# Performance work log

Hardware: AMD Instinct MI355X
Metric: run time of the kernel (lower is better)

The kernel has to match this reference:

```python
import jax, jax.numpy as jnp
import numpy as np

EPS = 1e-5
COMMIT_W = 2.0
LATENT = 64


def _conv1d(x, w, b, stride, padding):
    # x: [B,C,T], w: [O,I,K] (torch Conv1d layout)
    y = jax.lax.conv_general_dilated(x, w, (stride,), [(padding, padding)],
                                     dimension_numbers=('NCH', 'OIH', 'NCH'))
    return y + b[None, :, None]


def _bn(x, g, b):
    # training-mode BatchNorm1d: batch statistics over (B, T) per channel
    mu = x.mean(axis=(0, 2), keepdims=True)
    var = x.var(axis=(0, 2), keepdims=True)
    return (x - mu) * jax.lax.rsqrt(var + EPS) * g[None, :, None] + b[None, :, None]


def setup_inputs():
    key = jax.random.key(0)
    ks = jax.random.split(key, 10)
    B, T, D, K = 8, 10240, LATENT, 8192
    f32 = jnp.float32
    def n(k, shape, scale):
        return jax.random.normal(k, shape, dtype=f32) * scale
    return {
        'x': jax.random.normal(ks[0], (B, 1, T), dtype=f32),
        'enc_w1': n(ks[1], (16, 1, 5), 0.3), 'enc_b1': jnp.zeros((16,), f32),
        'bn1_g': jnp.ones((16,), f32), 'bn1_b': jnp.zeros((16,), f32),
        'enc_w2': n(ks[2], (32, 16, 5), 0.1), 'enc_b2': jnp.zeros((32,), f32),
        'bn2_g': jnp.ones((32,), f32), 'bn2_b': jnp.zeros((32,), f32),
        'enc_w3': n(ks[3], (64, 32, 25), 0.05), 'enc_b3': jnp.zeros((64,), f32),
        'bn3_g': jnp.ones((64,), f32), 'bn3_b': jnp.zeros((64,), f32),
        'codebook': jax.random.normal(ks[4], (K, D), dtype=f32),
        'dec_wt': n(ks[5], (64, 64, 25), 0.05),  # torch ConvTranspose1d [in,out,k]
        'dbn1_g': jnp.ones((64,), f32), 'dbn1_b': jnp.zeros((64,), f32),
        'dec_w2': n(ks[6], (64, 64, 5), 0.08), 'dec_b2': jnp.zeros((64,), f32),
        'dbn2_g': jnp.ones((64,), f32), 'dbn2_b': jnp.zeros((64,), f32),
        'dec_w3': n(ks[7], (1, 64, 1), 0.1), 'dec_b3': jnp.zeros((1,), f32),
    }


def reference(x, enc_w1, enc_b1, bn1_g, bn1_b, enc_w2, enc_b2, bn2_g, bn2_b,
              enc_w3, enc_b3, bn3_g, bn3_b, codebook, dec_wt, dbn1_g, dbn1_b,
              dec_w2, dec_b2, dbn2_g, dbn2_b, dec_w3, dec_b3):
    # ---- encoder ----
    h = jax.nn.silu(_conv1d(x, enc_w1, enc_b1, 1, 2))
    h = _bn(h, bn1_g, bn1_b)
    h = jax.nn.silu(_conv1d(h, enc_w2, enc_b2, 1, 2))
    h = _bn(h, bn2_g, bn2_b)
    h = jnp.tanh(_conv1d(h, enc_w3, enc_b3, 5, 12))
    z = _bn(h, bn3_g, bn3_b)                       # [B, 64, L]
    B, _, L = z.shape
    # ---- VQ: euclidean nearest-neighbor against codebook ----
    zf = z.transpose(0, 2, 1).reshape(-1, LATENT)  # [N, D]
    d = ((zf * zf).sum(-1, keepdims=True)
         - 2.0 * zf @ codebook.T
         + (codebook * codebook).sum(-1)[None, :])  # [N, K]
    idx = jnp.argmin(d, axis=-1)                   # [N]
    q = codebook[idx]                              # [N, D]
    commit_loss = COMMIT_W * jnp.mean((jax.lax.stop_gradient(q) - zf) ** 2)
    q_st = zf + jax.lax.stop_gradient(q - zf)      # straight-through
    zq = q_st.reshape(B, L, LATENT).transpose(0, 2, 1)  # [B, 64, L]
    # ---- decoder ----
    # ConvTranspose1d(k=25, s=5, p=12) == dilated conv with flipped kernel
    wconv = jnp.flip(dec_wt, -1).transpose(1, 0, 2)     # [out, in, k]
    h = jax.lax.conv_general_dilated(zq, wconv, (1,), [(12, 12)], lhs_dilation=(5,),
                                     dimension_numbers=('NCH', 'OIH', 'NCH'))
    h = jax.nn.silu(h)
    h = _bn(h, dbn1_g, dbn1_b)
    h = jax.nn.silu(_conv1d(h, dec_w2, dec_b2, 1, 2))
    h = _bn(h, dbn2_g, dbn2_b)
    recon = _conv1d(h, dec_w3, dec_b3, 1, 0)       # [B, 1, ~T]
    T = x.shape[2]
    cur = recon.shape[2]
    if cur > T:
        recon = recon[:, :, :T]
    elif cur < T:
        recon = jnp.pad(recon, ((0, 0), (0, 0), (0, T - cur)))
    return recon, idx.reshape(B, L), commit_loss
```

## Files before the change

### kernel.cpp

```cpp
#include <hip/hip_runtime.h>
#include <hip/hip_bf16.h>

#define DEV __device__ __forceinline__

typedef __attribute__((ext_vector_type(8))) short s8v;
typedef __attribute__((ext_vector_type(16))) float f32x16;
typedef __attribute__((address_space(1))) const unsigned int u32g;
typedef __attribute__((address_space(3))) unsigned int u32l;

DEV void gl_lds(const void* g, void* l){
  __builtin_amdgcn_global_load_lds((u32g*)g, (u32l*)l, 16, 0, 0);
}

DEV float siluf(float x){ return x / (1.f + expf(-x)); }

DEV float wredsum(float v){
  #pragma unroll
  for(int m = 32; m; m >>= 1) v += __shfl_xor(v, m);
  return v;
}

DEV unsigned short bf16rne(float f){
  unsigned int u = __float_as_uint(f);
  u += 0x7FFFu + ((u >> 16) & 1u);
  return (unsigned short)(u >> 16);
}
DEV float bf16tof(unsigned short h){ return __uint_as_float(((unsigned int)h) << 16); }

DEV unsigned umed3(unsigned a, unsigned b, unsigned c){
  unsigned d;
  asm("v_med3_u32 %0, %1, %2, %3" : "=v"(d) : "v"(a), "v"(b), "v"(c));
  return d;
}

#define S1 0
#define Q1 16
#define S2 32
#define Q2 64
#define S3 96
#define Q3 160
#define S4 224
#define Q4 288
#define S5 352
#define Q5 416
#define SLOSS 480
#define NSTATF 512

#define EPSQ 6u
#define NCHUNK 8

__global__ void k_prep(const float* ew3, const float* dwt, float* w3t, float* dwtt,
                       unsigned short* wb7){
  const int n1 = 64*32*25, n2 = 64*64*25;
  for(int i = blockIdx.x*blockDim.x + threadIdx.x; i < n1+n2; i += gridDim.x*blockDim.x){
    if(i < n1){
      int c = i/(32*25), r = i - c*(32*25), ii = r/25, k = r - ii*25;
      w3t[(ii*25 + k)*64 + c] = ew3[i];
    } else {
      int j = i - n1;
      int ii = j/(64*25), r = j - ii*(64*25), o = r/25, k = r - o*25;
      float w = dwt[j];
      dwtt[(ii*25 + k)*64 + o] = w;
      wb7[((size_t)(k*64 + o))*64 + ii] = bf16rne(w);
    }
  }
}

__global__ void k_prep2(const float* __restrict__ cb, unsigned short* __restrict__ cbsw,
                        float* __restrict__ cnw, float* __restrict__ cnw2,
                        unsigned short* __restrict__ cbb, int* cnt){
  if(blockIdx.x == 0 && threadIdx.x == 0) *cnt = 0;
  int j = blockIdx.x*256 + threadIdx.x;
  if(j < 8192){
    float nrm = 0.f;
    unsigned swz = (j & 15) << 4;
    char* rowp = (char*)cbsw + (size_t)j*256;
    #pragma unroll
    for(int k = 0; k < 64; k++){
      float x = cb[(size_t)j*64 + k];
      unsigned short hi = bf16rne(x);
      float lo = x - bf16tof(hi);
      *(unsigned short*)(rowp + (((unsigned)(2*k)) ^ swz)) = hi;
      *(unsigned short*)(rowp + (((unsigned)(128 + 2*k)) ^ swz)) = bf16rne(lo);
      cbb[(size_t)j*64 + k] = hi;
      nrm = fmaf(x, x, nrm);
    }
    cnw[j] = nrm;
    cnw2[j] = (nrm + 1024.f) * 256.f;
  }
}

__global__ void k1(const float* __restrict__ x, const float* __restrict__ w1,
                   const float* __restrict__ b1, float* __restrict__ h1, float* stats){
  __shared__ float xs[260];
  __shared__ float ssum[16], ssq[16];
  int tid = threadIdx.x, b = blockIdx.y, t0 = blockIdx.x*256;
  if(tid < 16){ ssum[tid] = 0.f; ssq[tid] = 0.f; }
  for(int i = tid; i < 260; i += 256){
    int t = t0 + i - 2;
    xs[i] = (t >= 0 && t < 10240) ? x[b*10240 + t] : 0.f;
  }
  __syncthreads();
  int t = t0 + tid;
  #pragma unroll
  for(int c = 0; c < 16; c++){
    float a = b1[c];
    #pragma unroll
    for(int k = 0; k < 5; k++) a = fmaf(w1[c*5+k], xs[tid+k], a);
    a = siluf(a);
    h1[((b*16 + c)*10240) + t] = a;
    float s = wredsum(a), s2 = wredsum(a*a);
    if((tid & 63) == 0){ atomicAdd(&ssum[c], s); atomicAdd(&ssq[c], s2); }
  }
  __syncthreads();
  if(tid < 16){ atomicAdd(stats+S1+tid, ssum[tid]); atomicAdd(stats+Q1+tid, ssq[tid]); }
}

__global__ void k2(const float* __restrict__ h1, const float* __restrict__ w2,
                   const float* __restrict__ b2, const float* __restrict__ g1,
                   const float* __restrict__ bb1, float* __restrict__ h2out, float* stats){
  __shared__ float hs[16*264];
  __shared__ float wl[2560];
  __shared__ float A1[16], B1[16];
  __shared__ float ssum[32], ssq[32];
  int tid = threadIdx.x, b = blockIdx.y, t0 = blockIdx.x*256;
  for(int i = tid; i < 2560; i += 256) wl[i] = w2[i];
  if(tid < 16){
    float mu = stats[S1+tid]/81920.f;
    float var = stats[Q1+tid]/81920.f - mu*mu;
    float rs = rsqrtf(var + 1e-5f);
    A1[tid] = rs*g1[tid];
    B1[tid] = bb1[tid] - mu*rs*g1[tid];
  }
  if(tid < 32){ ssum[tid] = 0.f; ssq[tid] = 0.f; }
  __syncthreads();
  for(int i = tid; i < 16*260; i += 256){
    int ch = i/260, tt = i - ch*260;
    int t = t0 + tt - 2;
    hs[ch*264 + tt] = (t >= 0 && t < 10240) ? (h1[((b*16+ch)*10240)+t]*A1[ch] + B1[ch]) : 0.f;
  }
  __syncthreads();
  int t = t0 + tid;
  float acc[32];
  #pragma unroll
  for(int c = 0; c < 32; c++) acc[c] = b2[c];
  for(int i = 0; i < 16; i++){
    float z0 = hs[i*264+tid], z1 = hs[i*264+tid+1], z2 = hs[i*264+tid+2],
          z3 = hs[i*264+tid+3], z4 = hs[i*264+tid+4];
    #pragma unroll
    for(int c = 0; c < 32; c++){
      const float* wp = &wl[(c*16+i)*5];
      acc[c] = fmaf(wp[0],z0,fmaf(wp[1],z1,fmaf(wp[2],z2,fmaf(wp[3],z3,fmaf(wp[4],z4,acc[c])))));
    }
  }
  #pragma unroll
  for(int c = 0; c < 32; c++){
    float a = siluf(acc[c]);
    h2out[((b*32 + c)*10240) + t] = a;
    float s = wredsum(a), s2 = wredsum(a*a);
    if((tid & 63) == 0){ atomicAdd(&ssum[c], s); atomicAdd(&ssq[c], s2); }
  }
  __syncthreads();
  if(tid < 32){ atomicAdd(stats+S2+tid, ssum[tid]); atomicAdd(stats+Q2+tid, ssq[tid]); }
}

__global__ void k3(const float* __restrict__ h2, const float* __restrict__ w3t,
                   const float* __restrict__ eb3, const float* __restrict__ g2,
                   const float* __restrict__ bb2, float* __restrict__ zn, float* stats){
  __shared__ float X[5*32*40];
  __shared__ float A2[32], B2[32];
  __shared__ float ssum[64], ssq[64];
  int tid = threadIdx.x, b = blockIdx.y, l0 = blockIdx.x*32;
  if(tid < 32){
    float mu = stats[S2+tid]/81920.f;
    float var = stats[Q2+tid]/81920.f - mu*mu;
    float rs = rsqrtf(var + 1e-5f);
    A2[tid] = rs*g2[tid];
    B2[tid] = bb2[tid] - mu*rs*g2[tid];
  }
  if(tid < 64){ ssum[tid] = 0.f; ssq[tid] = 0.f; }
  __syncthreads();
  for(int i2 = tid; i2 < 5*32*36; i2 += 256){
    int kk = i2/(32*36);
    int r  = i2 - kk*(32*36);
    int ch = r/36, m = r - ch*36;
    int t = 5*(l0 + m) + kk - 12;
    float v = 0.f;
    if(t >= 0 && t < 10240) v = h2[((b*32+ch)*10240)+t]*A2[ch] + B2[ch];
    X[(kk*32+ch)*40 + m] = v;
  }
  __syncthreads();
  int c = tid & 63, lslot = tid >> 6;
  float acc[8];
  float bias = eb3[c];
  #pragma unroll
  for(int s = 0; s < 8; s++) acc[s] = bias;
  for(int i = 0; i < 32; i++){
    #pragma unroll
    for(int kk = 0; kk < 5; kk++){
      float z[12];
      #pragma unroll
      for(int j = 0; j < 12; j++) z[j] = X[(kk*32+i)*40 + lslot*8 + j];
      #pragma unroll
      for(int kap = 0; kap < 5; kap++){
        float w = w3t[(i*25 + kap*5 + kk)*64 + c];
        #pragma unroll
        for(int s = 0; s < 8; s++) acc[s] = fmaf(w, z[s+kap], acc[s]);
      }
    }
  }
  float ls = 0.f, lq = 0.f;
  #pragma unroll
  for(int s = 0; s < 8; s++){
    int l = l0 + lslot*8 + s;
    float a = tanhf(acc[s]);
    zn[((b*2048 + l)*64) + c] = a;
    ls += a; lq += a*a;
  }
  atomicAdd(&ssum[c], ls); atomicAdd(&ssq[c], lq);
  __syncthreads();
  if(tid < 64){ atomicAdd(stats+S3+tid, ssum[tid]); atomicAdd(stats+Q3+tid, ssq[tid]); }
}

__global__ void k3b(float* zn, const float* g3, const float* b3, const float* stats){
  __shared__ float A[64], B[64];
  int tid = threadIdx.x;
  if(tid < 64){
    float mu = stats[S3+tid]/16384.f;
    float var = stats[Q3+tid]/16384.f - mu*mu;
    float rs = rsqrtf(var + 1e-5f);
    A[tid] = rs*g3[tid];
    B[tid] = b3[tid] - mu*rs*g3[tid];
  }
  __syncthreads();
  for(int i = blockIdx.x*256 + tid; i < 16384*64; i += gridDim.x*256){
    int c = i & 63;
    zn[i] = zn[i]*A[c] + B[c];
  }
}

__global__ __launch_bounds__(256, 3) void k5m(const float* __restrict__ zn,
    const unsigned short* __restrict__ cbsw, const float* __restrict__ cnw2,
    unsigned int* __restrict__ pbk, unsigned int* __restrict__ psk){
  __shared__ __align__(16) unsigned char cbuf[2][16384];
  __shared__ unsigned int redb[64][2], reds[64][2];
  int tid = threadIdx.x;
  int chunk = blockIdx.x;
  int m0 = blockIdx.y * 64;
  int lane = tid & 63, widx = tid >> 6;
  int wr = widx >> 1, wc = widx & 1;
  int h = lane >> 5;
  int row = m0 + wr*32 + (lane & 31);

  s8v ah[4], al[4];
  const float* zp = zn + (size_t)row*64;
  #pragma unroll
  for(int s = 0; s < 4; s++){
    float4 v0 = *(const float4*)(zp + s*16 + h*8);
    float4 v1 = *(const float4*)(zp + s*16 + h*8 + 4);
    float vv[8] = {v0.x,v0.y,v0.z,v0.w,v1.x,v1.y,v1.z,v1.w};
    #pragma unroll
    for(int i = 0; i < 8; i++){
      unsigned short hi = bf16rne(vv[i]);
      ah[s][i] = (short)hi;
      al[s][i] = (short)bf16rne(vv[i] - bf16tof(hi));
    }
  }

  unsigned int bk[16], sk[16];
  #pragma unroll
  for(int r = 0; r < 16; r++){ bk[r] = 0xFFFFFFFFu; sk[r] = 0xFFFFFFFFu; }
  f32x16 zv;
  #pragma unroll
  for(int i = 0; i < 16; i++) zv[i] = 0.f;

  int c0 = chunk * 1024;
  const char* csrc = (const char*)cbsw + (size_t)c0*256;
  #pragma unroll
  for(int c2 = 0; c2 < 4; c2++)
    gl_lds(csrc + c2*4096 + tid*16, &cbuf[0][0] + c2*4096 + tid*16);
  __syncthreads();

  int cl = wc*32 + (lane & 31);
  unsigned swz = (unsigned)(cl & 15) << 4;
  unsigned col = (unsigned)(c0 + cl);
  for(int tile = 0; tile < 16; ++tile){
    int bsel = tile & 1;
    if(tile < 15){
      const char* ns = csrc + (size_t)(tile+1)*16384;
      #pragma unroll
      for(int c2 = 0; c2 < 4; c2++)
        gl_lds(ns + c2*4096 + tid*16, &cbuf[bsel^1][0] + c2*4096 + tid*16);
    }
    const unsigned char* bp = &cbuf[bsel][0] + cl*256;
    s8v bh[4], bl[4];
    #pragma unroll
    for(int s = 0; s < 4; s++){
      bh[s] = *(const s8v*)(bp + (((unsigned)(s*32 + h*16)) ^ swz));
      bl[s] = *(const s8v*)(bp + (((unsigned)(128 + s*32 + h*16)) ^ swz));
    }
    float cnv2 = cnw2[col];
    f32x16 a1 = __builtin_amdgcn_mfma_f32_32x32x16_bf16(ah[0], bh[0], zv, 0, 0, 0);
    f32x16 a2 = __builtin_amdgcn_mfma_f32_32x32x16_bf16(al[0], bh[0], zv, 0, 0, 0);
    a2 = __builtin_amdgcn_mfma_f32_32x32x16_bf16(ah[0], bl[0], a2, 0, 0, 0);
    #pragma unroll
    for(int s = 1; s < 4; s++){
      a1 = __builtin_amdgcn_mfma_f32_32x32x16_bf16(ah[s], bh[s], a1, 0, 0, 0);
      a2 = __builtin_amdgcn_mfma_f32_32x32x16_bf16(al[s], bh[s], a2, 0, 0, 0);
      a2 = __builtin_amdgcn_mfma_f32_32x32x16_bf16(ah[s], bl[s], a2, 0, 0, 0);
    }
    #pragma unroll
    for(int r = 0; r < 16; r++){
      float q = fmaf(-512.f, a1[r], cnv2);
      q = fmaf(-512.f, a2[r], q);
      q = fminf(q, 524287.f);
      unsigned k = (((unsigned)q) << 13) | col;
      unsigned nb = bk[r] < k ? bk[r] : k;
      sk[r] = umed3(sk[r], bk[r], k);
      bk[r] = nb;
    }
    col += 64;
    __syncthreads();
  }

  #pragma unroll
  for(int m = 1; m <= 16; m <<= 1){
    #pragma unroll
    for(int r = 0; r < 16; r++){
      unsigned int ob = (unsigned int)__shfl_xor((int)bk[r], m);
      unsigned int os = (unsigned int)__shfl_xor((int)sk[r], m);
      unsigned int s2 = sk[r] < os ? sk[r] : os;
      sk[r] = umed3(s2, bk[r], ob);
      bk[r] = bk[r] < ob ? bk[r] : ob;
    }
  }
  if((lane & 31) == 0){
    #pragma unroll
    for(int r = 0; r < 16; r++){
      int lr = wr*32 + (r&3) + 8*(r>>2) + 4*h;
      redb[lr][wc] = bk[r]; reds[lr][wc] = sk[r];
    }
  }
  __syncthreads();
  if(tid < 64){
    unsigned int b0 = redb[tid][0], b1v = redb[tid][1];
    unsigned int s0 = reds[tid][0], s1v = reds[tid][1];
    unsigned int ss = s0 < s1v ? s0 : s1v;
    ss = umed3(ss, b0, b1v);
    unsigned int bb = b0 < b1v ? b0 : b1v;
    size_t o = (size_t)chunk*16384 + m0 + tid;
    pbk[o] = bb;
    psk[o] = ss;
  }
}

__global__ void k5r(const unsigned int* __restrict__ pbk,
                    const unsigned int* __restrict__ psk, int* __restrict__ idxw,
                    float* __restrict__ out_idx, int* __restrict__ list, int* cnt){
  int row = blockIdx.x*256 + threadIdx.x;
  unsigned int bk = pbk[row], sk = psk[row];
  #pragma unroll
  for(int c = 1; c < NCHUNK; c++){
    unsigned int ob = pbk[(size_t)c*16384 + row];
    unsigned int os = psk[(size_t)c*16384 + row];
    unsigned int s2 = sk < os ? sk : os;
    sk = umed3(s2, bk, ob);
    bk = bk < ob ? bk : ob;
  }
  int idx = (int)(bk & 0x1FFFu);
  idxw[row] = idx;
  out_idx[row] = (float)idx;
  if((sk >> 13) - (bk >> 13) <= EPSQ){
    int p = atomicAdd(cnt, 1);
    list[p] = row;
  }
}

__global__ __launch_bounds__(256) void k5x(const float* __restrict__ zn,
    const float* __restrict__ cb, const float* __restrict__ cnw,
    const int* __restrict__ list, const int* cnt,
    float* __restrict__ pxd, int* __restrict__ pxi){
  int tid = threadIdx.x;
  int chunk = blockIdx.x;
  int n = *cnt;
  int rgrp = tid >> 6, cs = tid & 63;
  int c0 = chunk * 1024;
  for(int bat = blockIdx.y; bat*4 < n; bat += 256){
    int e = bat*4 + rgrp;
    int ec = e < n ? e : n-1;
    int row = list[ec];
    float4 zr[16];
    const float4* zp = (const float4*)(zn + (size_t)row*64);
    #pragma unroll
    for(int q = 0; q < 16; q++) zr[q] = zp[q];
    float bd = 3.4e38f; int bi = 0;
    for(int step = 0; step < 16; step++){
      int j = c0 + step*64 + cs;
      const float4* cp = (const float4*)(cb + (size_t)j*64);
      float cnv = cnw[j];
      float da = 0.f, db = 0.f;
      #pragma unroll
      for(int q = 0; q < 16; q += 2){
        float4 ca = cp[q], cb4 = cp[q+1];
        da = fmaf(ca.x, zr[q].x, da);  da = fmaf(ca.y, zr[q].y, da);
        da = fmaf(ca.z, zr[q].z, da);  da = fmaf(ca.w, zr[q].w, da);
        db = fmaf(cb4.x, zr[q+1].x, db); db = fmaf(cb4.y, zr[q+1].y, db);
        db = fmaf(cb4.z, zr[q+1].z, db); db = fmaf(cb4.w, zr[q+1].w, db);
      }
      float d = fmaf(-2.f, da + db, cnv);
      if(d < bd){ bd = d; bi = j; }
    }
    #pragma unroll
    for(int m = 1; m <= 32; m <<= 1){
      float od = __shfl_xor(bd, m);
      int   oi = __shfl_xor(bi, m);
      if(od < bd || (od == bd && oi < bi)){ bd = od; bi = oi; }
    }
    if(cs == 0 && e < n){
      pxd[(size_t)chunk*16384 + e] = bd;
      pxi[(size_t)chunk*16384 + e] = bi;
    }
  }
}

__global__ void k5x2(const float* __restrict__ pxd, const int* __restrict__ pxi,
                     const int* __restrict__ list, const int* cnt,
                     int* __restrict__ idxw, float* __restrict__ out_idx){
  int e = blockIdx.x*256 + threadIdx.x;
  int n = *cnt;
  if(e >= n) return;
  float bd = pxd[e]; int bi = pxi[e];
  #pragma unroll
  for(int c = 1; c < NCHUNK; c++){
    float od = pxd[(size_t)c*16384 + e];
    int   oi = pxi[(size_t)c*16384 + e];
    if(od < bd || (od == bd && oi < bi)){ bd = od; bi = oi; }
  }
  int row = list[e];
  idxw[row] = bi;
  out_idx[row] = (float)bi;
}

__global__ void k_loss(const float* __restrict__ zn, const float* __restrict__ cb,
                       const int* __restrict__ idxw, float* stats){
  int row = blockIdx.x*256 + threadIdx.x;
  int code = idxw[row];
  const float* cp = cb + (size_t)code*64;
  const float* zp = zn + (size_t)row*64;
  float s = 0.f;
  #pragma unroll
  for(int k = 0; k < 64; k++){
    float dd = cp[k] - zp[k];
    s = fmaf(dd, dd, s);
  }
  float tot = wredsum(s);
  if((threadIdx.x & 63) == 0) atomicAdd(stats + SLOSS, tot);
}

__global__ void k6(const float* stats, float* out){
  if(threadIdx.x == 0) out[0] = 2.f * stats[SLOSS] / 1048576.f;
}

__global__ void k7z(unsigned int* __restrict__ h4t){
  for(int i = threadIdx.x; i < 3072; i += 256){
    int b = i / 384, r = i - b*384;
    int row12 = r >> 5, word = r & 31;
    int row = row12 < 2 ? row12 : 10236 + row12;
    h4t[((size_t)b*10248 + row)*32 + word] = 0u;
  }
}

__global__ __launch_bounds__(320) void k7m(const int* __restrict__ idxp,
    const unsigned short* __restrict__ cbb, const unsigned short* __restrict__ wb7,
    unsigned short* __restrict__ h4t, float* stats){
  __shared__ __align__(16) unsigned char lA[37*128];
  __shared__ float tb[5*64*33];
  __shared__ float ssum[64], ssq[64];
  int tid = threadIdx.x, b = blockIdx.y, u0 = blockIdx.x*32;
  if(tid < 64){ ssum[tid] = 0.f; ssq[tid] = 0.f; }
  {
    int m = tid >> 3, part = tid & 7;
    if(m < 37){
      int u = u0 - 2 + m;
      uint4 val = make_uint4(0,0,0,0);
      if(u >= 0 && u < 2048){
        int code = idxp[b*2048 + u];
        val = *(const uint4*)((const char*)cbb + (size_t)code*128 + part*16);
      }
      *(uint4*)(lA + m*128 + (((unsigned)(part*16)) ^ (((unsigned)m & 7) << 4))) = val;
    }
  }
  __syncthreads();
  int lane = tid & 63, h = lane >> 5, cl = lane & 31;
  int v = tid >> 6;
  const int km[5]  = {2,3,4,0,1};
  const int ovv[5] = {2,2,2,3,3};
  f32x16 acc0, acc1;
  #pragma unroll
  for(int i = 0; i < 16; i++){ acc0[i] = 0.f; acc1[i] = 0.f; }
  #pragma unroll
  for(int r = 0; r < 5; r++){
    int off = ovv[v] - r + 2;
    int m = cl + off;
    unsigned aswz = ((unsigned)m & 7) << 4;
    int k = km[v] + 5*r;
    const char* b0p = (const char*)wb7 + (size_t)(k*64 + cl)*128;
    const char* b1p = b0p + 32*128;
    #pragma unroll
    for(int s = 0; s < 4; s++){
      unsigned o = (unsigned)(s*32 + h*16);
      s8v a  = *(const s8v*)(lA + m*128 + (o ^ aswz));
      s8v b0 = *(const s8v*)(b0p + o);
      s8v b1 = *(const s8v*)(b1p + o);
      acc0 = __builtin_amdgcn_mfma_f32_32x32x16_bf16(a, b0, acc0, 0, 0, 0);
      acc1 = __builtin_amdgcn_mfma_f32_32x32x16_bf16(a, b1, acc1, 0, 0, 0);
    }
  }
  float ps0 = 0.f, pq0 = 0.f, ps1 = 0.f, pq1 = 0.f;
  #pragma unroll
  for(int r = 0; r < 16; r++){
    int ul = (r&3) + 8*(r>>2) + 4*h;
    int u = u0 + ul;
    float v0 = siluf(acc0[r]), v1 = siluf(acc1[r]);
    tb[(v*64 + cl)*33 + ul]      = v0;
    tb[(v*64 + 32 + cl)*33 + ul] = v1;
    if(v == 0 || u < 2047){ ps0 += v0; pq0 += v0*v0; ps1 += v1; pq1 += v1*v1; }
  }
  atomicAdd(&ssum[cl], ps0);      atomicAdd(&ssq[cl], pq0);
  atomicAdd(&ssum[32 + cl], ps1); atomicAdd(&ssq[32 + cl], pq1);
  __syncthreads();
  if(tid < 64){ atomicAdd(stats+S4+tid, ssum[tid]); atomicAdd(stats+Q4+tid, ssq[tid]); }
  #pragma unroll
  for(int j = 0; j < 16; j++){
    int flat = j*320 + tid;
    int tl = flat >> 5;
    int chp = flat & 31;
    int t = u0*5 + tl;
    if(t < 10236){
      int vv = tl % 5, ul = tl / 5;
      float f0 = tb[(vv*64 + 2*chp)*33 + ul];
      float f1 = tb[(vv*64 + 2*chp + 1)*33 + ul];
      unsigned int pk = (unsigned int)bf16rne(f0) | ((unsigned int)bf16rne(f1) << 16);
      size_t rowb = ((size_t)b*10248 + 2 + t)*128;
      *(unsigned int*)((char*)h4t + rowb + (((unsigned)(4*chp)) ^ (((unsigned)t & 7) << 4))) = pk;
    }
  }
}

__global__ void k8w(const float* __restrict__ w2d, const float* __restrict__ b2d,
                    const float* __restrict__ g4, const float* __restrict__ bb4,
                    const float* __restrict__ stats, unsigned short* __restrict__ wbt,
                    float* __restrict__ beta){
  __shared__ float A4[64], B4[64];
  int tid = threadIdx.x;
  if(tid < 64){
    float mu = stats[S4+tid]/81888.f;
    float var = stats[Q4+tid]/81888.f - mu*mu;
    float rs = rsqrtf(var + 1e-5f);
    A4[tid] = rs*g4[tid];
    B4[tid] = bb4[tid] - mu*rs*g4[tid];
  }
  __syncthreads();
  for(int e = tid; e < 64*64*5; e += 256){
    int c = e/320, r = e - c*320, i = r/5, k = r - i*5;
    unsigned short hw = bf16rne(w2d[e] * A4[i]);
    int row = k*64 + c;
    *(unsigned short*)((char*)wbt + (size_t)row*128 + (((unsigned)(2*i)) ^ (((unsigned)c & 7) << 4))) = hw;
  }
  if(tid < 64){
    float s = b2d[tid];
    for(int i = 0; i < 64; i++){
      float wsum = 0.f;
      #pragma unroll
      for(int k = 0; k < 5; k++) wsum += w2d[(tid*64 + i)*5 + k];
      s += wsum * B4[i];
    }
    beta[tid] = s;
  }
}

__global__ __launch_bounds__(256) void k8(const unsigned short* __restrict__ h4t,
    const unsigned short* __restrict__ wbt, const float* __restrict__ beta,
    unsigned short* __restrict__ h5b, float* stats){
  __shared__ __align__(16) unsigned char lA[17408];
  __shared__ __align__(16) unsigned char lB[40960];
  __shared__ float ssum[64], ssq[64];
  int tid = threadIdx.x, b = blockIdx.y, t0 = blockIdx.x*128;
  if(tid < 64){ ssum[tid] = 0.f; ssq[tid] = 0.f; }
  #pragma unroll
  for(int c2 = 0; c2 < 10; c2++)
    gl_lds((const char*)wbt + c2*4096 + tid*16, lB + c2*4096 + tid*16);
  const char* srcA = (const char*)h4t + ((size_t)b*10248 + t0)*128;
  #pragma unroll
  for(int c2 = 0; c2 < 4; c2++)
    gl_lds(srcA + c2*4096 + tid*16, lA + c2*4096 + tid*16);
  if(tid < 64) gl_lds(srcA + 16384 + tid*16, lA + 16384 + tid*16);
  __syncthreads();

  int lane = tid & 63, h = lane >> 5, cl = lane & 31;
  int wt0 = (tid >> 6) * 32;
  f32x16 acc0, acc1;
  #pragma unroll
  for(int i = 0; i < 16; i++){ acc0[i] = 0.f; acc1[i] = 0.f; }
  unsigned bswz = (unsigned)(cl & 7) << 4;
  #pragma unroll
  for(int k = 0; k < 5; k++){
    int l = wt0 + cl + k;
    unsigned aswz = (unsigned)((l + 6) & 7) << 4;
    int arow = l*128;
    int brow = (k*64 + cl)*128;
    #pragma unroll
    for(int s = 0; s < 4; s++){
      unsigned o = (unsigned)(s*32 + h*16);
      s8v a  = *(const s8v*)(lA + arow + (o ^ aswz));
      s8v b0 = *(const s8v*)(lB + brow + (o ^ bswz));
      s8v b1 = *(const s8v*)(lB + brow + 4096 + (o ^ bswz));
      acc0 = __builtin_amdgcn_mfma_f32_32x32x16_bf16(a, b0, acc0, 0, 0, 0);
      acc1 = __builtin_amdgcn_mfma_f32_32x32x16_bf16(a, b1, acc1, 0, 0, 0);
    }
  }
  float bet0 = beta[cl], bet1 = beta[32 + cl];
  float ps0 = 0.f, pq0 = 0.f, ps1 = 0.f, pq1 = 0.f;
  #pragma unroll
  for(int r = 0; r < 16; r++){
    int t = t0 + wt0 + (r&3) + 8*(r>>2) + 4*h;
    float v0 = siluf(acc0[r] + bet0);
    float v1 = siluf(acc1[r] + bet1);
    if(t < 10236){
      size_t o = ((size_t)b*10240 + t)*64;
      h5b[o + cl]      = bf16rne(v0);
      h5b[o + 32 + cl] = bf16rne(v1);
      ps0 += v0; pq0 += v0*v0; ps1 += v1; pq1 += v1*v1;
    }
  }
  atomicAdd(&ssum[cl], ps0);      atomicAdd(&ssq[cl], pq0);
  atomicAdd(&ssum[32 + cl], ps1); atomicAdd(&ssq[32 + cl], pq1);
  __syncthreads();
  if(tid < 64){ atomicAdd(stats+S5+tid, ssum[tid]); atomicAdd(stats+Q5+tid, ssq[tid]); }
}

__global__ void k9(const unsigned short* __restrict__ h5b, const float* __restrict__ w3,
                   const float* __restrict__ b3, const float* __restrict__ g5,
                   const float* __restrict__ bb5, const float* stats,
                   float* __restrict__ out){
  __shared__ float WA[64], WB[64];
  int tid = threadIdx.x;
  if(tid < 64){
    float mu = stats[S5+tid]/81888.f;
    float var = stats[Q5+tid]/81888.f - mu*mu;
    float rs = rsqrtf(var + 1e-5f);
    float A = rs*g5[tid], B = bb5[tid] - mu*rs*g5[tid];
    float w = w3[tid];
    WA[tid] = w*A; WB[tid] = w*B;
  }
  __syncthreads();
  int b = blockIdx.y;
  int t = blockIdx.x*256 + tid;
  float acc = b3[0];
  if(t < 10236){
    const unsigned short* hp = h5b + ((size_t)b*10240 + t)*64;
    #pragma unroll
    for(int q = 0; q < 8; q++){
      uint4 u = *(const uint4*)(hp + q*8);
      unsigned int ua[4] = {u.x, u.y, u.z, u.w};
      #pragma unroll
      for(int w = 0; w < 4; w++){
        int c = q*8 + w*2;
        acc += WA[c]*bf16tof((unsigned short)(ua[w] & 0xFFFFu)) + WB[c];
        acc += WA[c+1]*bf16tof((unsigned short)(ua[w] >> 16)) + WB[c+1];
      }
    }
  } else acc = 0.f;
  out[b*10240 + t] = acc;
}

extern "C" void kernel_launch(void* const* d_in, const int* in_sizes, int n_in,
                              void* d_out, int out_size, void* d_ws, size_t ws_size,
                              hipStream_t stream){
  const float* x   = (const float*)d_in[0];
  const float* ew1 = (const float*)d_in[1];
  const float* eb1 = (const float*)d_in[2];
  const float* g1  = (const float*)d_in[3];
  const float* bb1 = (const float*)d_in[4];
  const float* ew2 = (const float*)d_in[5];
  const float* eb2 = (const float*)d_in[6];
  const float* g2  = (const float*)d_in[7];
  const float* bb2 = (const float*)d_in[8];
  const float* ew3 = (const float*)d_in[9];
  const float* eb3 = (const float*)d_in[10];
  const float* g3  = (const float*)d_in[11];
  const float* bb3 = (const float*)d_in[12];
  const float* cb  = (const float*)d_in[13];
  const float* dwt = (const float*)d_in[14];
  const float* g4  = (const float*)d_in[15];
  const float* bb4 = (const float*)d_in[16];
  const float* w2d = (const float*)d_in[17];
  const float* b2d = (const float*)d_in[18];
  const float* g5  = (const float*)d_in[19];
  const float* bb5 = (const float*)d_in[20];
  const float* w3d = (const float*)d_in[21];
  const float* b3d = (const float*)d_in[22];

  char* ws = (char*)d_ws;
  float* h1   = (float*)(ws + 0);
  unsigned short* cbsw = (unsigned short*)(ws + 0);
  float* cnw  = (float*)(ws + 2097152);
  float* cnw2 = (float*)(ws + 2129920);
  float* h2   = (float*)(ws + 5242880);
  float* zn   = (float*)(ws + 15728640);
  unsigned short* h4t = (unsigned short*)(ws + 0);
  unsigned short* h5b = (unsigned short*)(ws + 20971520);
  int*   list = (int*)  (ws + 20971520);
  int*   cnt  = (int*)  (ws + 21037056);
  unsigned int* pbk = (unsigned int*)(ws + 21037312);
  unsigned int* psk = (unsigned int*)(ws + 21561600);
  float* pxd  = (float*)(ws + 22085888);
  int*   pxi  = (int*)  (ws + 22610176);
  unsigned short* wbt = (unsigned short*)(ws + 31457280);
  float* beta = (float*)(ws + 31498240);
  unsigned short* wb7 = (unsigned short*)(ws + 32000000);
  unsigned short* cbb = (unsigned short*)(ws + 32300032);
  float* w3t  = (float*)(ws + 41934848);
  float* dwtt = (float*)(ws + 42139648);
  int*   idxw = (int*)  (ws + 42549248);
  float* stats= (float*)(ws + 42614784);
  if(ws_size < 42616832) return;

  float* out = (float*)d_out;

  hipMemsetAsync(stats, 0, NSTATF*4, stream);
  k_prep<<<600, 256, 0, stream>>>(ew3, dwt, w3t, dwtt, wb7);
  k1<<<dim3(40,8), 256, 0, stream>>>(x, ew1, eb1, h1, stats);
  k2<<<dim3(40,8), 256, 0, stream>>>(h1, ew2, eb2, g1, bb1, h2, stats);
  k_prep2<<<32, 256, 0, stream>>>(cb, cbsw, cnw, cnw2, cbb, cnt);
  k3<<<dim3(64,8), 256, 0, stream>>>(h2, w3t, eb3, g2, bb2, zn, stats);
  k3b<<<1024, 256, 0, stream>>>(zn, g3, bb3, stats);
  k5m<<<dim3(NCHUNK,256), 256, 0, stream>>>(zn, cbsw, cnw2, pbk, psk);
  k5r<<<64, 256, 0, stream>>>(pbk, psk, idxw, out + 81920, list, cnt);
  k5x<<<dim3(NCHUNK,256), 256, 0, stream>>>(zn, cb, cnw, list, cnt, pxd, pxi);
  k5x2<<<64, 256, 0, stream>>>(pxd, pxi, list, cnt, idxw, out + 81920);
  k_loss<<<64, 256, 0, stream>>>(zn, cb, idxw, stats);
  k6<<<1, 64, 0, stream>>>(stats, out + 98304);
  k7z<<<1, 256, 0, stream>>>((unsigned int*)h4t);
  k7m<<<dim3(64,8), 320, 0, stream>>>(idxw, cbb, wb7, h4t, stats);
  k8w<<<1, 256, 0, stream>>>(w2d, b2d, g4, bb4, stats, wbt, beta);
  k8<<<dim3(80,8), 256, 0, stream>>>(h4t, wbt, beta, h5b, stats);
  k9<<<dim3(40,8), 256, 0, stream>>>(h5b, w3d, b3d, g5, bb5, stats, out);
}
```

Measured before the change: 407.1 us.

## Retile k3, k5m and k8, and fold tiny k6/k7z launches into neighbors

k3 now covers 16 latent positions per block instead of 32, doubling the grid and shrinking its LDS and register footprint, with float4 LDS reads. In k5m each wave now scans all 64 codebook columns of a tile for its own 32 rows, so a block covers 128 rows. This doubles reuse of each staged codebook tile and removes the cross-wave LDS reduction. k8 moves to 64-timestep blocks with one accumulator per wave and reads weights straight from global memory instead of staging them in LDS. The single-thread k6 loss write and the k7z padding zeroing are merged into k9 and k8w, removing two launches; the risk is more global or L2 weight traffic in k8 and lower occupancy from k5m's larger row tile.

```diff
diff --git a/kernel.cpp b/kernel.cpp
--- a/kernel.cpp
+++ b/kernel.cpp
@@ -167,10 +167,10 @@
 __global__ void k3(const float* __restrict__ h2, const float* __restrict__ w3t,
                    const float* __restrict__ eb3, const float* __restrict__ g2,
                    const float* __restrict__ bb2, float* __restrict__ zn, float* stats){
-  __shared__ float X[5*32*40];
+  __shared__ __align__(16) float X[5*32*24];
   __shared__ float A2[32], B2[32];
   __shared__ float ssum[64], ssq[64];
-  int tid = threadIdx.x, b = blockIdx.y, l0 = blockIdx.x*32;
+  int tid = threadIdx.x, b = blockIdx.y, l0 = blockIdx.x*16;
   if(tid < 32){
     float mu = stats[S2+tid]/81920.f;
     float var = stats[Q2+tid]/81920.f - mu*mu;
@@ -180,39 +180,40 @@
   }
   if(tid < 64){ ssum[tid] = 0.f; ssq[tid] = 0.f; }
   __syncthreads();
-  for(int i2 = tid; i2 < 5*32*36; i2 += 256){
-    int kk = i2/(32*36);
-    int r  = i2 - kk*(32*36);
-    int ch = r/36, m = r - ch*36;
+  for(int i2 = tid; i2 < 5*32*20; i2 += 256){
+    int kk = i2/640;
+    int r  = i2 - kk*640;
+    int ch = r/20, m = r - ch*20;
     int t = 5*(l0 + m) + kk - 12;
     float v = 0.f;
     if(t >= 0 && t < 10240) v = h2[((b*32+ch)*10240)+t]*A2[ch] + B2[ch];
-    X[(kk*32+ch)*40 + m] = v;
+    X[(kk*32+ch)*24 + m] = v;
   }
   __syncthreads();
   int c = tid & 63, lslot = tid >> 6;
-  float acc[8];
+  float acc[4];
   float bias = eb3[c];
   #pragma unroll
-  for(int s = 0; s < 8; s++) acc[s] = bias;
+  for(int s = 0; s < 4; s++) acc[s] = bias;
   for(int i = 0; i < 32; i++){
     #pragma unroll
     for(int kk = 0; kk < 5; kk++){
-      float z[12];
-      #pragma unroll
-      for(int j = 0; j < 12; j++) z[j] = X[(kk*32+i)*40 + lslot*8 + j];
+      const float* xp = &X[(kk*32+i)*24 + lslot*4];
+      float4 za = *(const float4*)(xp);
+      float4 zb = *(const float4*)(xp + 4);
+      float z[8] = {za.x,za.y,za.z,za.w,zb.x,zb.y,zb.z,zb.w};
       #pragma unroll
       for(int kap = 0; kap < 5; kap++){
         float w = w3t[(i*25 + kap*5 + kk)*64 + c];
         #pragma unroll
-        for(int s = 0; s < 8; s++) acc[s] = fmaf(w, z[s+kap], acc[s]);
+        for(int s = 0; s < 4; s++) acc[s] = fmaf(w, z[s+kap], acc[s]);
       }
     }
   }
   float ls = 0.f, lq = 0.f;
   #pragma unroll
-  for(int s = 0; s < 8; s++){
-    int l = l0 + lslot*8 + s;
+  for(int s = 0; s < 4; s++){
+    int l = l0 + lslot*4 + s;
     float a = tanhf(acc[s]);
     zn[((b*2048 + l)*64) + c] = a;
     ls += a; lq += a*a;
@@ -243,14 +244,12 @@
     const unsigned short* __restrict__ cbsw, const float* __restrict__ cnw2,
     unsigned int* __restrict__ pbk, unsigned int* __restrict__ psk){
   __shared__ __align__(16) unsigned char cbuf[2][16384];
-  __shared__ unsigned int redb[64][2], reds[64][2];
   int tid = threadIdx.x;
   int chunk = blockIdx.x;
-  int m0 = blockIdx.y * 64;
-  int lane = tid & 63, widx = tid >> 6;
-  int wr = widx >> 1, wc = widx & 1;
-  int h = lane >> 5;
-  int row = m0 + wr*32 + (lane & 31);
+  int m0 = blockIdx.y * 128;
+  int lane = tid & 63, wr = tid >> 6;
+  int h = lane >> 5, cll = lane & 31;
+  int row = m0 + wr*32 + cll;
 
   s8v ah[4], al[4];
   const float* zp = zn + (size_t)row*64;
@@ -281,9 +280,7 @@
     gl_lds(csrc + c2*4096 + tid*16, &cbuf[0][0] + c2*4096 + tid*16);
   __syncthreads();
 
-  int cl = wc*32 + (lane & 31);
-  unsigned swz = (unsigned)(cl & 15) << 4;
-  unsigned col = (unsigned)(c0 + cl);
+  unsigned swz = (unsigned)(cll & 15) << 4;
   for(int tile = 0; tile < 16; ++tile){
     int bsel = tile & 1;
     if(tile < 15){
@@ -292,34 +289,37 @@
       for(int c2 = 0; c2 < 4; c2++)
         gl_lds(ns + c2*4096 + tid*16, &cbuf[bsel^1][0] + c2*4096 + tid*16);
     }
-    const unsigned char* bp = &cbuf[bsel][0] + cl*256;
-    s8v bh[4], bl[4];
-    #pragma unroll
-    for(int s = 0; s < 4; s++){
-      bh[s] = *(const s8v*)(bp + (((unsigned)(s*32 + h*16)) ^ swz));
-      bl[s] = *(const s8v*)(bp + (((unsigned)(128 + s*32 + h*16)) ^ swz));
-    }
-    float cnv2 = cnw2[col];
-    f32x16 a1 = __builtin_amdgcn_mfma_f32_32x32x16_bf16(ah[0], bh[0], zv, 0, 0, 0);
-    f32x16 a2 = __builtin_amdgcn_mfma_f32_32x32x16_bf16(al[0], bh[0], zv, 0, 0, 0);
-    a2 = __builtin_amdgcn_mfma_f32_32x32x16_bf16(ah[0], bl[0], a2, 0, 0, 0);
-    #pragma unroll
-    for(int s = 1; s < 4; s++){
-      a1 = __builtin_amdgcn_mfma_f32_32x32x16_bf16(ah[s], bh[s], a1, 0, 0, 0);
-      a2 = __builtin_amdgcn_mfma_f32_32x32x16_bf16(al[s], bh[s], a2, 0, 0, 0);
-      a2 = __builtin_amdgcn_mfma_f32_32x32x16_bf16(ah[s], bl[s], a2, 0, 0, 0);
-    }
-    #pragma unroll
-    for(int r = 0; r < 16; r++){
-      float q = fmaf(-512.f, a1[r], cnv2);
-      q = fmaf(-512.f, a2[r], q);
-      q = fminf(q, 524287.f);
-      unsigned k = (((unsigned)q) << 13) | col;
-      unsigned nb = bk[r] < k ? bk[r] : k;
-      sk[r] = umed3(sk[r], bk[r], k);
-      bk[r] = nb;
-    }
-    col += 64;
+    #pragma unroll
+    for(int half = 0; half < 2; half++){
+      const unsigned char* bp = &cbuf[bsel][0] + (half*32 + cll)*256;
+      s8v bh[4], bl[4];
+      #pragma unroll
+      for(int s = 0; s < 4; s++){
+        bh[s] = *(const s8v*)(bp + (((unsigned)(s*32 + h*16)) ^ swz));
+        bl[s] = *(const s8v*)(bp + (((unsigned)(128 + s*32 + h*16)) ^ swz));
+      }
+      unsigned col = (unsigned)(c0 + tile*64 + half*32 + cll);
+      float cnv2 = cnw2[col];
+      f32x16 a1 = __builtin_amdgcn_mfma_f32_32x32x16_bf16(ah[0], bh[0], zv, 0, 0, 0);
+      f32x16 a2 = __builtin_amdgcn_mfma_f32_32x32x16_bf16(al[0], bh[0], zv, 0, 0, 0);
+      a2 = __builtin_amdgcn_mfma_f32_32x32x16_bf16(ah[0], bl[0], a2, 0, 0, 0);
+      #pragma unroll
+      for(int s = 1; s < 4; s++){
+        a1 = __builtin_amdgcn_mfma_f32_32x32x16_bf16(ah[s], bh[s], a1, 0, 0, 0);
+        a2 = __builtin_amdgcn_mfma_f32_32x32x16_bf16(al[s], bh[s], a2, 0, 0, 0);
+        a2 = __builtin_amdgcn_mfma_f32_32x32x16_bf16(ah[s], bl[s], a2, 0, 0, 0);
+      }
+      #pragma unroll
+      for(int r = 0; r < 16; r++){
+        float q = fmaf(-512.f, a1[r], cnv2);
+        q = fmaf(-512.f, a2[r], q);
+        q = fminf(q, 524287.f);
+        unsigned k = (((unsigned)q) << 13) | col;
+        unsigned nb = bk[r] < k ? bk[r] : k;
+        sk[r] = umed3(sk[r], bk[r], k);
+        bk[r] = nb;
+      }
+    }
     __syncthreads();
   }
 
@@ -334,23 +334,14 @@
       bk[r] = bk[r] < ob ? bk[r] : ob;
     }
   }
-  if((lane & 31) == 0){
+  if(cll == 0){
+    size_t base = (size_t)chunk*16384 + m0 + wr*32 + 4*h;
     #pragma unroll
     for(int r = 0; r < 16; r++){
-      int lr = wr*32 + (r&3) + 8*(r>>2) + 4*h;
-      redb[lr][wc] = bk[r]; reds[lr][wc] = sk[r];
-    }
-  }
-  __syncthreads();
-  if(tid < 64){
-    unsigned int b0 = redb[tid][0], b1v = redb[tid][1];
-    unsigned int s0 = reds[tid][0], s1v = reds[tid][1];
-    unsigned int ss = s0 < s1v ? s0 : s1v;
-    ss = umed3(ss, b0, b1v);
-    unsigned int bb = b0 < b1v ? b0 : b1v;
-    size_t o = (size_t)chunk*16384 + m0 + tid;
-    pbk[o] = bb;
-    psk[o] = ss;
+      int lr = (r&3) + 8*(r>>2);
+      pbk[base + lr] = bk[r];
+      psk[base + lr] = sk[r];
+    }
   }
 }
 
@@ -455,19 +446,6 @@
   }
   float tot = wredsum(s);
   if((threadIdx.x & 63) == 0) atomicAdd(stats + SLOSS, tot);
-}
-
-__global__ void k6(const float* stats, float* out){
-  if(threadIdx.x == 0) out[0] = 2.f * stats[SLOSS] / 1048576.f;
-}
-
-__global__ void k7z(unsigned int* __restrict__ h4t){
-  for(int i = threadIdx.x; i < 3072; i += 256){
-    int b = i / 384, r = i - b*384;
-    int row12 = r >> 5, word = r & 31;
-    int row = row12 < 2 ? row12 : 10236 + row12;
-    h4t[((size_t)b*10248 + row)*32 + word] = 0u;
-  }
 }
 
 __global__ __launch_bounds__(320) void k7m(const int* __restrict__ idxp,
@@ -550,9 +528,15 @@
 __global__ void k8w(const float* __restrict__ w2d, const float* __restrict__ b2d,
                     const float* __restrict__ g4, const float* __restrict__ bb4,
                     const float* __restrict__ stats, unsigned short* __restrict__ wbt,
-                    float* __restrict__ beta){
+                    float* __restrict__ beta, unsigned int* __restrict__ h4tz){
   __shared__ float A4[64], B4[64];
   int tid = threadIdx.x;
+  for(int i = tid; i < 3072; i += 256){
+    int b = i / 384, r = i - b*384;
+    int row12 = r >> 5, word = r & 31;
+    int row = row12 < 2 ? row12 : 10236 + row12;
+    h4tz[((size_t)b*10248 + row)*32 + word] = 0u;
+  }
   if(tid < 64){
     float mu = stats[S4+tid]/81888.f;
     float var = stats[Q4+tid]/81888.f - mu*mu;
@@ -582,59 +566,50 @@
 __global__ __launch_bounds__(256) void k8(const unsigned short* __restrict__ h4t,
     const unsigned short* __restrict__ wbt, const float* __restrict__ beta,
     unsigned short* __restrict__ h5b, float* stats){
-  __shared__ __align__(16) unsigned char lA[17408];
-  __shared__ __align__(16) unsigned char lB[40960];
+  __shared__ __align__(16) unsigned char lA[68*128];
   __shared__ float ssum[64], ssq[64];
-  int tid = threadIdx.x, b = blockIdx.y, t0 = blockIdx.x*128;
+  int tid = threadIdx.x, b = blockIdx.y, t0 = blockIdx.x*64;
   if(tid < 64){ ssum[tid] = 0.f; ssq[tid] = 0.f; }
-  #pragma unroll
-  for(int c2 = 0; c2 < 10; c2++)
-    gl_lds((const char*)wbt + c2*4096 + tid*16, lB + c2*4096 + tid*16);
   const char* srcA = (const char*)h4t + ((size_t)b*10248 + t0)*128;
   #pragma unroll
-  for(int c2 = 0; c2 < 4; c2++)
+  for(int c2 = 0; c2 < 2; c2++)
     gl_lds(srcA + c2*4096 + tid*16, lA + c2*4096 + tid*16);
-  if(tid < 64) gl_lds(srcA + 16384 + tid*16, lA + 16384 + tid*16);
+  if(tid < 32) gl_lds(srcA + 8192 + tid*16, lA + 8192 + tid*16);
   __syncthreads();
 
   int lane = tid & 63, h = lane >> 5, cl = lane & 31;
-  int wt0 = (tid >> 6) * 32;
-  f32x16 acc0, acc1;
-  #pragma unroll
-  for(int i = 0; i < 16; i++){ acc0[i] = 0.f; acc1[i] = 0.f; }
+  int widx = tid >> 6;
+  int wt0 = (widx >> 1) * 32;
+  int wch = (widx & 1) * 32;
+  f32x16 acc;
+  #pragma unroll
+  for(int i = 0; i < 16; i++) acc[i] = 0.f;
   unsigned bswz = (unsigned)(cl & 7) << 4;
   #pragma unroll
   for(int k = 0; k < 5; k++){
     int l = wt0 + cl + k;
     unsigned aswz = (unsigned)((l + 6) & 7) << 4;
-    int arow = l*128;
-    int brow = (k*64 + cl)*128;
+    const char* bp = (const char*)wbt + (size_t)(k*64 + wch + cl)*128;
     #pragma unroll
     for(int s = 0; s < 4; s++){
       unsigned o = (unsigned)(s*32 + h*16);
-      s8v a  = *(const s8v*)(lA + arow + (o ^ aswz));
-      s8v b0 = *(const s8v*)(lB + brow + (o ^ bswz));
-      s8v b1 = *(const s8v*)(lB + brow + 4096 + (o ^ bswz));
-      acc0 = __builtin_amdgcn_mfma_f32_32x32x16_bf16(a, b0, acc0, 0, 0, 0);
-      acc1 = __builtin_amdgcn_mfma_f32_32x32x16_bf16(a, b1, acc1, 0, 0, 0);
-    }
-  }
-  float bet0 = beta[cl], bet1 = beta[32 + cl];
-  float ps0 = 0.f, pq0 = 0.f, ps1 = 0.f, pq1 = 0.f;
+      s8v a  = *(const s8v*)(lA + l*128 + (o ^ aswz));
+      s8v bb = *(const s8v*)(bp + (o ^ bswz));
+      acc = __builtin_amdgcn_mfma_f32_32x32x16_bf16(a, bb, acc, 0, 0, 0);
+    }
+  }
+  float bet = beta[wch + cl];
+  float ps = 0.f, pq = 0.f;
   #pragma unroll
   for(int r = 0; r < 16; r++){
     int t = t0 + wt0 + (r&3) + 8*(r>>2) + 4*h;
-    float v0 = siluf(acc0[r] + bet0);
-    float v1 = siluf(acc1[r] + bet1);
+    float v0 = siluf(acc[r] + bet);
     if(t < 10236){
-      size_t o = ((size_t)b*10240 + t)*64;
-      h5b[o + cl]      = bf16rne(v0);
-      h5b[o + 32 + cl] = bf16rne(v1);
-      ps0 += v0; pq0 += v0*v0; ps1 += v1; pq1 += v1*v1;
-    }
-  }
-  atomicAdd(&ssum[cl], ps0);      atomicAdd(&ssq[cl], pq0);
-  atomicAdd(&ssum[32 + cl], ps1); atomicAdd(&ssq[32 + cl], pq1);
+      h5b[((size_t)b*10240 + t)*64 + wch + cl] = bf16rne(v0);
+      ps += v0; pq += v0*v0;
+    }
+  }
+  atomicAdd(&ssum[wch + cl], ps); atomicAdd(&ssq[wch + cl], pq);
   __syncthreads();
   if(tid < 64){ atomicAdd(stats+S5+tid, ssum[tid]); atomicAdd(stats+Q5+tid, ssq[tid]); }
 }
@@ -645,6 +620,8 @@
                    float* __restrict__ out){
   __shared__ float WA[64], WB[64];
   int tid = threadIdx.x;
+  if(blockIdx.x == 0 && blockIdx.y == 0 && tid == 0)
+    out[98304] = 2.f * stats[SLOSS] / 1048576.f;
   if(tid < 64){
     float mu = stats[S5+tid]/81888.f;
     float var = stats[Q5+tid]/81888.f - mu*mu;
@@ -733,17 +710,15 @@
   k1<<<dim3(40,8), 256, 0, stream>>>(x, ew1, eb1, h1, stats);
   k2<<<dim3(40,8), 256, 0, stream>>>(h1, ew2, eb2, g1, bb1, h2, stats);
   k_prep2<<<32, 256, 0, stream>>>(cb, cbsw, cnw, cnw2, cbb, cnt);
-  k3<<<dim3(64,8), 256, 0, stream>>>(h2, w3t, eb3, g2, bb2, zn, stats);
+  k3<<<dim3(128,8), 256, 0, stream>>>(h2, w3t, eb3, g2, bb2, zn, stats);
   k3b<<<1024, 256, 0, stream>>>(zn, g3, bb3, stats);
-  k5m<<<dim3(NCHUNK,256), 256, 0, stream>>>(zn, cbsw, cnw2, pbk, psk);
+  k5m<<<dim3(NCHUNK,128), 256, 0, stream>>>(zn, cbsw, cnw2, pbk, psk);
   k5r<<<64, 256, 0, stream>>>(pbk, psk, idxw, out + 81920, list, cnt);
   k5x<<<dim3(NCHUNK,256), 256, 0, stream>>>(zn, cb, cnw, list, cnt, pxd, pxi);
   k5x2<<<64, 256, 0, stream>>>(pxd, pxi, list, cnt, idxw, out + 81920);
   k_loss<<<64, 256, 0, stream>>>(zn, cb, idxw, stats);
-  k6<<<1, 64, 0, stream>>>(stats, out + 98304);
-  k7z<<<1, 256, 0, stream>>>((unsigned int*)h4t);
   k7m<<<dim3(64,8), 320, 0, stream>>>(idxw, cbb, wb7, h4t, stats);
-  k8w<<<1, 256, 0, stream>>>(w2d, b2d, g4, bb4, stats, wbt, beta);
-  k8<<<dim3(80,8), 256, 0, stream>>>(h4t, wbt, beta, h5b, stats);
+  k8w<<<1, 256, 0, stream>>>(w2d, b2d, g4, bb4, stats, wbt, beta, (unsigned int*)h4t);
+  k8<<<dim3(160,8), 256, 0, stream>>>(h4t, wbt, beta, h5b, stats);
   k9<<<dim3(40,8), 256, 0, stream>>>(h5b, w3d, b3d, g5, bb5, stats, out);
 }
```

After: 389.0 us. -4.4%, faster.
